# Optimization experiments

Hardware: AMD Instinct MI355X
Metric: run time of the kernel (lower is better)

## Reference

```python
import jax, jax.numpy as jnp
import numpy as np

N_NODES = 100000
N_EDGES = 3200000
IN_CH = 256
HID = 256   # 2 * out_channels
OUT = 128


def _gcn_norm(edge_index, n):
    # PyG GCNConv normalization: add self-loops, norm = d^-1/2[src] * d^-1/2[dst]
    src, dst = edge_index[0], edge_index[1]
    loops = jnp.arange(n, dtype=src.dtype)
    src = jnp.concatenate([src, loops])
    dst = jnp.concatenate([dst, loops])
    ones = jnp.ones_like(dst, dtype=jnp.float32)
    deg = jax.ops.segment_sum(ones, dst, num_segments=n)
    dinv = jnp.where(deg > 0, jax.lax.rsqrt(deg), 0.0)
    norm = dinv[src] * dinv[dst]
    return src, dst, norm


def _gcn_conv(x, W, b, src, dst, norm, n):
    h = x @ W                              # [N, F_out] dense transform first (F_out <= F_in)
    msg = h[src] * norm[:, None]           # gather + scale  [E+N, F_out]
    out = jax.ops.segment_sum(msg, dst, num_segments=n)  # scatter-add
    return out + b


def setup_inputs() -> dict:
    key = jax.random.key(0)
    k1, k2, k3, k4 = jax.random.split(key, 4)
    x = jax.random.normal(k1, (N_NODES, IN_CH), dtype=jnp.float32)
    edge_index = jax.random.randint(k2, (2, N_EDGES), 0, N_NODES, dtype=jnp.int64)
    # Glorot-style init for weights, zero bias (PyG GCNConv defaults)
    W1 = jax.random.normal(k3, (IN_CH, HID), dtype=jnp.float32) * (1.0 / np.sqrt(IN_CH))
    b1 = jnp.zeros((HID,), dtype=jnp.float32)
    W2 = jax.random.normal(k4, (HID, OUT), dtype=jnp.float32) * (1.0 / np.sqrt(HID))
    b2 = jnp.zeros((OUT,), dtype=jnp.float32)
    return {"x": x, "edge_index": edge_index, "W1": W1, "b1": b1, "W2": W2, "b2": b2}


def reference(x, edge_index, W1, b1, W2, b2):
    n = x.shape[0]
    src, dst, norm = _gcn_norm(edge_index, n)  # cached=True: shared across both layers
    h = _gcn_conv(x, W1, b1, src, dst, norm, n)
    h = jax.nn.relu(h)
    z = _gcn_conv(h, W2, b2, src, dst, norm, n)
    return z
```

## Files before the change

kernel.cpp:

```cpp
#include <hip/hip_runtime.h>
#include <cstdio>


#define NPB 256
#define PCHUNK 8192

typedef _Float16 half4v __attribute__((ext_vector_type(4)));
typedef _Float16 half8v __attribute__((ext_vector_type(8)));
typedef float    f32x4  __attribute__((ext_vector_type(4)));
typedef float    f32x8  __attribute__((ext_vector_type(8)));

__global__ __launch_bounds__(256) void k_bhist(const int* __restrict__ dst,
                                               int* __restrict__ bcnt,
                                               int e, int nb) {
  __shared__ int h[512];
  for (int i = threadIdx.x; i < nb; i += 256) h[i] = 0;
  __syncthreads();
  int c0 = blockIdx.x * PCHUNK;
  int c1 = min(c0 + PCHUNK, e);
  for (int i = c0 + threadIdx.x; i < c1; i += 256)
    atomicAdd(&h[dst[i] >> 8], 1);
  __syncthreads();
  for (int i = threadIdx.x; i < nb; i += 256)
    if (h[i]) atomicAdd(&bcnt[i], h[i]);
}

__global__ __launch_bounds__(512) void k_bscan(const int* __restrict__ bcnt,
                                               int* __restrict__ bbase,
                                               int* __restrict__ gcur, int nb) {
  __shared__ int sm[512];
  int tid = threadIdx.x;
  sm[tid] = (tid < nb) ? bcnt[tid] : 0;
  __syncthreads();
  for (int d = 1; d < 512; d <<= 1) {
    int t = (tid >= d) ? sm[tid - d] : 0;
    __syncthreads();
    sm[tid] += t;
    __syncthreads();
  }
  int ex = (tid == 0) ? 0 : sm[tid - 1];
  if (tid < nb) {
    bbase[tid] = ex;
    gcur[tid] = ex;
  }
  if (tid == nb) bbase[nb] = sm[nb - 1];
}

__global__ __launch_bounds__(256) void k_partition(const int* __restrict__ src,
                                                   const int* __restrict__ dst,
                                                   int* __restrict__ gcur,
                                                   uint2* __restrict__ tmp,
                                                   int e, int nb) {
  __shared__ int hist[512];
  __shared__ int base[512];
  for (int i = threadIdx.x; i < nb; i += 256) hist[i] = 0;
  __syncthreads();
  int c0 = blockIdx.x * PCHUNK;
  int c1 = min(c0 + PCHUNK, e);
  for (int i = c0 + threadIdx.x; i < c1; i += 256)
    atomicAdd(&hist[dst[i] >> 8], 1);
  __syncthreads();
  for (int i = threadIdx.x; i < nb; i += 256) {
    int c = hist[i];
    base[i] = c ? atomicAdd(&gcur[i], c) : 0;
    hist[i] = 0;
  }
  __syncthreads();
  for (int i = c0 + threadIdx.x; i < c1; i += 256) {
    int d = dst[i];
    int b = d >> 8;
    int pos = base[b] + atomicAdd(&hist[b], 1);
    uint2 v;
    v.x = (unsigned)src[i];
    v.y = (unsigned)d;
    tmp[pos] = v;
  }
}

__global__ __launch_bounds__(256) void k_bucket(const uint2* __restrict__ tmp,
                                                const int* __restrict__ bbase,
                                                int* __restrict__ off,
                                                float* __restrict__ dinv,
                                                int* __restrict__ esrc, int n) {
  __shared__ int lcnt[NPB];
  __shared__ int lsum[NPB];
  __shared__ int lcur[NPB];
  const int b = blockIdx.x;
  const int tid = threadIdx.x;
  const int r0 = b << 8;
  const int nn = min(NPB, n - r0);
  const int lo = bbase[b], hi = bbase[b + 1];

  lcnt[tid] = 0;
  __syncthreads();
  for (int i = lo + tid; i < hi; i += 256)
    atomicAdd(&lcnt[tmp[i].y & (NPB - 1)], 1);
  __syncthreads();
  lsum[tid] = lcnt[tid];
  __syncthreads();
  for (int d = 1; d < NPB; d <<= 1) {
    int t = (tid >= d) ? lsum[tid - d] : 0;
    __syncthreads();
    lsum[tid] += t;
    __syncthreads();
  }
  int ex = (tid == 0) ? 0 : lsum[tid - 1];
  if (tid < nn) {
    off[r0 + tid] = lo + ex;
    dinv[r0 + tid] = rsqrtf((float)(lcnt[tid] + 1));
    lcur[tid] = lo + ex;
  }
  if (r0 + nn == n && tid == 0) off[n] = hi;
  __syncthreads();
  for (int i = lo + tid; i < hi; i += 256) {
    uint2 t2 = tmp[i];
    int pos = atomicAdd(&lcur[t2.y & (NPB - 1)], 1);
    esrc[pos] = (int)t2.x;
  }
}

__global__ __launch_bounds__(256) void k_castWT(const float* __restrict__ W,
                                                _Float16* __restrict__ WhT,
                                                _Float16* __restrict__ WlT,
                                                int K, int N) {
  int i = blockIdx.x * 256 + threadIdx.x;
  if (i >= K * N) return;
  int n = i % N, k = i / N;
  float v = W[i];
  _Float16 h = (_Float16)v;
  WhT[(size_t)n * K + k] = h;
  WlT[(size_t)n * K + k] = (_Float16)(v - (float)h);
}

__global__ __launch_bounds__(256, 2) void k_gemm1(
    const float* __restrict__ A, const _Float16* __restrict__ BhT,
    const _Float16* __restrict__ BlT, _Float16* __restrict__ C,
    int M, int N, int K) {
  __shared__ _Float16 Ah[128][40];
  __shared__ _Float16 Al[128][40];

  const int tid = threadIdx.x;
  const int bm = blockIdx.x * 128;

  const int arow = tid >> 1;
  const int acol = (tid & 1) * 16;
  const bool avalid = (bm + arow) < M;
  const float* aptr = A + (size_t)(bm + arow) * K + acol;

  const int wave = tid >> 6, lane = tid & 63;
  const int wm = (wave & 1) * 64, wn = (wave >> 1) * 128;
  const int lr = lane & 15, quad = lane >> 4;

  const _Float16* bh0 = BhT + (size_t)(wn + lr) * K + quad * 8;
  const _Float16* bl0 = BlT + (size_t)(wn + lr) * K + quad * 8;

  f32x4 acc[4][8] = {};

  for (int k0 = 0; k0 < K; k0 += 32) {
    __syncthreads();
    if (avalid) {
#pragma unroll
      for (int ii = 0; ii < 4; ++ii) {
        f32x4 v = *(const f32x4*)(aptr + k0 + ii * 4);
        half4v hv, lv;
#pragma unroll
        for (int j = 0; j < 4; ++j) {
          hv[j] = (_Float16)v[j];
          lv[j] = (_Float16)(v[j] - (float)hv[j]);
        }
        *(half4v*)&Ah[arow][acol + ii * 4] = hv;
        *(half4v*)&Al[arow][acol + ii * 4] = lv;
      }
    } else {
      half4v z = {};
#pragma unroll
      for (int ii = 0; ii < 4; ++ii) {
        *(half4v*)&Ah[arow][acol + ii * 4] = z;
        *(half4v*)&Al[arow][acol + ii * 4] = z;
      }
    }
    __syncthreads();

    half8v af[4], alf[4];
#pragma unroll
    for (int mi = 0; mi < 4; ++mi) {
      af[mi] = *(const half8v*)&Ah[wm + mi * 16 + lr][quad * 8];
      alf[mi] = *(const half8v*)&Al[wm + mi * 16 + lr][quad * 8];
    }
#pragma unroll
    for (int ni = 0; ni < 8; ++ni) {
      half8v bh = *(const half8v*)(bh0 + (size_t)(ni * 16) * K + k0);
      half8v bl = *(const half8v*)(bl0 + (size_t)(ni * 16) * K + k0);
#pragma unroll
      for (int mi = 0; mi < 4; ++mi) {
        acc[mi][ni] = __builtin_amdgcn_mfma_f32_16x16x32_f16(
            af[mi], bh, acc[mi][ni], 0, 0, 0);
        acc[mi][ni] = __builtin_amdgcn_mfma_f32_16x16x32_f16(
            af[mi], bl, acc[mi][ni], 0, 0, 0);
        acc[mi][ni] = __builtin_amdgcn_mfma_f32_16x16x32_f16(
            alf[mi], bh, acc[mi][ni], 0, 0, 0);
      }
    }
  }

#pragma unroll
  for (int mi = 0; mi < 4; ++mi)
#pragma unroll
    for (int r = 0; r < 4; ++r) {
      int row = bm + wm + mi * 16 + quad * 4 + r;
      if (row < M) {
#pragma unroll
        for (int ni = 0; ni < 8; ++ni)
          C[(size_t)row * N + wn + ni * 16 + lr] = (_Float16)acc[mi][ni][r];
      }
    }
}

template <typename AT, int NTERMS>
__global__ __launch_bounds__(256, 2) void k_gemm_mfma(
    const AT* __restrict__ A, const _Float16* __restrict__ BhT,
    const _Float16* __restrict__ BlT, _Float16* __restrict__ C,
    int M, int N, int K) {
  constexpr bool SPLITA = (NTERMS == 3);
  __shared__ _Float16 Ah[128][40];
  __shared__ _Float16 Al[SPLITA ? 128 : 1][40];

  const int tid = threadIdx.x;
  const int bm = blockIdx.x * 128;
  const int bn = blockIdx.y * 128;

  const int arow = tid >> 1;
  const int acol = (tid & 1) * 16;
  const bool avalid = (bm + arow) < M;
  const AT* aptr = A + (size_t)(bm + arow) * K + acol;

  const int wave = tid >> 6, lane = tid & 63;
  const int wm = (wave & 1) * 64, wn = (wave >> 1) * 64;
  const int lr = lane & 15, quad = lane >> 4;

  const _Float16* bh0 = BhT + (size_t)(bn + wn + lr) * K + quad * 8;
  const _Float16* bl0 = BlT + (size_t)(bn + wn + lr) * K + quad * 8;

  f32x4 acc[4][4] = {};

  for (int k0 = 0; k0 < K; k0 += 32) {
    __syncthreads();
    if (avalid) {
#pragma unroll
      for (int ii = 0; ii < 4; ++ii) {
        if constexpr (SPLITA) {
          f32x4 v = *(const f32x4*)(aptr + k0 + ii * 4);
          half4v hv, lv;
#pragma unroll
          for (int j = 0; j < 4; ++j) {
            hv[j] = (_Float16)v[j];
            lv[j] = (_Float16)(v[j] - (float)hv[j]);
          }
          *(half4v*)&Ah[arow][acol + ii * 4] = hv;
          *(half4v*)&Al[arow][acol + ii * 4] = lv;
        } else {
          half4v v = *(const half4v*)(aptr + k0 + ii * 4);
          *(half4v*)&Ah[arow][acol + ii * 4] = v;
        }
      }
    } else {
      half4v z = {};
#pragma unroll
      for (int ii = 0; ii < 4; ++ii) {
        *(half4v*)&Ah[arow][acol + ii * 4] = z;
        if constexpr (SPLITA) *(half4v*)&Al[arow][acol + ii * 4] = z;
      }
    }
    __syncthreads();

    half8v af[4], alf[4], bhf[4], blf[4];
#pragma unroll
    for (int mi = 0; mi < 4; ++mi) {
      af[mi] = *(const half8v*)&Ah[wm + mi * 16 + lr][quad * 8];
      if constexpr (SPLITA)
        alf[mi] = *(const half8v*)&Al[wm + mi * 16 + lr][quad * 8];
    }
#pragma unroll
    for (int ni = 0; ni < 4; ++ni) {
      bhf[ni] = *(const half8v*)(bh0 + (size_t)(ni * 16) * K + k0);
      blf[ni] = *(const half8v*)(bl0 + (size_t)(ni * 16) * K + k0);
    }
#pragma unroll
    for (int mi = 0; mi < 4; ++mi)
#pragma unroll
      for (int ni = 0; ni < 4; ++ni) {
        acc[mi][ni] = __builtin_amdgcn_mfma_f32_16x16x32_f16(
            af[mi], bhf[ni], acc[mi][ni], 0, 0, 0);
        acc[mi][ni] = __builtin_amdgcn_mfma_f32_16x16x32_f16(
            af[mi], blf[ni], acc[mi][ni], 0, 0, 0);
        if constexpr (SPLITA)
          acc[mi][ni] = __builtin_amdgcn_mfma_f32_16x16x32_f16(
              alf[mi], bhf[ni], acc[mi][ni], 0, 0, 0);
      }
  }

#pragma unroll
  for (int mi = 0; mi < 4; ++mi)
#pragma unroll
    for (int r = 0; r < 4; ++r) {
      int row = bm + wm + mi * 16 + quad * 4 + r;
      if (row < M) {
#pragma unroll
        for (int ni = 0; ni < 4; ++ni)
          C[(size_t)row * N + bn + wn + ni * 16 + lr] =
              (_Float16)acc[mi][ni][r];
      }
    }
}

template <int C, bool RELU, typename OutT>
__global__ __launch_bounds__(256) void k_agg(const _Float16* __restrict__ h,
                                             const int* __restrict__ esrc,
                                             const int* __restrict__ off,
                                             const float* __restrict__ dinv,
                                             const float* __restrict__ bias,
                                             OutT* __restrict__ out, int n) {
  constexpr int LPE = C / 8;
  constexpr int EPL = 64 / LPE;
  constexpr int U = 4;
  int gwave = (blockIdx.x * 256 + threadIdx.x) >> 6;
  int lane = threadIdx.x & 63;
  if (gwave >= n) return;
  const int i = gwave;
  const int eslot = lane / LPE;
  const int sub = lane % LPE;
  const float di = dinv[i];
  const _Float16* hb = h + sub * 8;

  f32x8 acc = {};
  if (eslot == 0)
    acc = di * __builtin_convertvector(*(const half8v*)(hb + (size_t)i * C),
                                       f32x8);

  int e = off[i];
  const int e1 = off[i + 1];
  for (; e + U * EPL <= e1; e += U * EPL) {
    int s[U];
#pragma unroll
    for (int g = 0; g < U; ++g) s[g] = esrc[e + g * EPL + eslot];
    float w[U];
    half8v v[U];
#pragma unroll
    for (int g = 0; g < U; ++g) {
      w[g] = dinv[s[g]];
      v[g] = *(const half8v*)(hb + (size_t)s[g] * C);
    }
#pragma unroll
    for (int g = 0; g < U; ++g)
      acc += w[g] * __builtin_convertvector(v[g], f32x8);
  }
  for (; e < e1; e += EPL) {
    int eg = e + eslot;
    if (eg < e1) {
      int s = esrc[eg];
      acc += dinv[s] * __builtin_convertvector(
                           *(const half8v*)(hb + (size_t)s * C), f32x8);
    }
  }

#pragma unroll
  for (int j = 0; j < 8; ++j) {
    float t = acc[j];
#pragma unroll
    for (int m = LPE; m < 64; m <<= 1) t += __shfl_xor(t, m);
    acc[j] = t;
  }

  if (eslot == 0) {
    f32x8 bv = *(const f32x8*)(bias + sub * 8);
    f32x8 r = acc * di + bv;
    if (RELU) {
#pragma unroll
      for (int j = 0; j < 8; ++j) r[j] = fmaxf(r[j], 0.f);
    }
    if constexpr (sizeof(OutT) == 2) {
      *(half8v*)(out + (size_t)i * C + sub * 8) =
          __builtin_convertvector(r, half8v);
    } else {
      *(f32x8*)(out + (size_t)i * C + sub * 8) = r;
    }
  }
}

extern "C" void kernel_launch(void* const* d_in, const int* in_sizes, int n_in,
                              void* d_out, int out_size, void* d_ws, size_t ws_size,
                              hipStream_t stream) {
  const float* x  = (const float*)d_in[0];
  const int*   ei = (const int*)d_in[1];
  const float* W1 = (const float*)d_in[2];
  const float* b1 = (const float*)d_in[3];
  const float* W2 = (const float*)d_in[4];
  const float* b2 = (const float*)d_in[5];
  float* out = (float*)d_out;

  const int IN_CH = 256, HID = 256, OUT = 128;
  const int N = in_sizes[0] / IN_CH;
  const int E = in_sizes[1] / 2;
  const int* src = ei;
  const int* dst = ei + E;
  const int NB = (N + NPB - 1) / NPB;

  char* p = (char*)d_ws;
  auto alloc = [&](size_t bytes) {
    void* r = (void*)p;
    p += (bytes + 255) & ~(size_t)255;
    return r;
  };
  _Float16* h1   = (_Float16*)alloc((size_t)N * HID * 2);
  _Float16* h1r  = (_Float16*)alloc((size_t)N * HID * 2);
  int*      esrc = (int*)alloc((size_t)E * 4);
  uint2*    tmp  = (uint2*)alloc((size_t)E * 8);
  int*      off  = (int*)alloc((size_t)(N + 1) * 4);
  float*    dinv = (float*)alloc((size_t)N * 4);
  int*      bcnt = (int*)alloc((size_t)(NB + 1) * 4);
  int*      bbase= (int*)alloc((size_t)(NB + 1) * 4);
  int*      gcur = (int*)alloc((size_t)(NB + 1) * 4);
  _Float16* w1h  = (_Float16*)alloc((size_t)IN_CH * HID * 2);
  _Float16* w1l  = (_Float16*)alloc((size_t)IN_CH * HID * 2);
  _Float16* w2h  = (_Float16*)alloc((size_t)HID * OUT * 2);
  _Float16* w2l  = (_Float16*)alloc((size_t)HID * OUT * 2);
  if ((size_t)(p - (char*)d_ws) > ws_size) {
    fprintf(stderr, "kernel_launch: ws too small (need %zu, have %zu)\n",
            (size_t)(p - (char*)d_ws), ws_size);
    return;
  }

  const int nBlkP = (E + PCHUNK - 1) / PCHUNK;

  hipMemsetAsync(bcnt, 0, (size_t)(NB + 1) * 4, stream);
  k_bhist<<<nBlkP, 256, 0, stream>>>(dst, bcnt, E, NB);
  k_bscan<<<1, 512, 0, stream>>>(bcnt, bbase, gcur, NB);
  k_partition<<<nBlkP, 256, 0, stream>>>(src, dst, gcur, tmp, E, NB);
  k_bucket<<<NB, 256, 0, stream>>>(tmp, bbase, off, dinv, esrc, N);
  k_castWT<<<(IN_CH * HID + 255) / 256, 256, 0, stream>>>(W1, w1h, w1l, IN_CH, HID);
  k_castWT<<<(HID * OUT + 255) / 256, 256, 0, stream>>>(W2, w2h, w2l, HID, OUT);
  k_gemm1<<<(N + 127) / 128, 256, 0, stream>>>(x, w1h, w1l, h1, N, HID, IN_CH);
  int aggBlk = (N + 3) / 4;
  k_agg<256, true, _Float16><<<aggBlk, 256, 0, stream>>>(h1, esrc, off, dinv, b1, h1r, N);
  dim3 g2((N + 127) / 128, OUT / 128);
  k_gemm_mfma<_Float16, 2><<<g2, 256, 0, stream>>>(h1r, w2h, w2l, h1, N, OUT, HID);
  k_agg<128, false, float><<<aggBlk, 256, 0, stream>>>(h1, esrc, off, dinv, b2, out, N);
}
```

Baseline: 744.3 us.

## Slice edges by source range and aggregate per slice for gather locality

Edges are bucketed by source-node slice (4096 nodes) and destination block, so each slice gets its own CSR offsets. The aggregation kernel gives each wave 33 destination nodes and walks slice by slice, so the gathered source rows in each phase fall in a narrow range that should stay in cache. The wide feature dimension is split into two 128-channel passes, with each lane handling two channels. In exchange the edge-sorting histograms get much larger (about 12.5K shared-memory bins) and per-edge parallelism drops, since each lane walks edges serially with short-vector loads.

```diff
diff --git a/kernel.cpp b/kernel.cpp
--- a/kernel.cpp
+++ b/kernel.cpp
@@ -4,33 +4,45 @@
 
 #define NPB 256
 #define PCHUNK 8192
-
+#define SLICE_SHIFT 12
+#define MAXB 12544
+
+typedef _Float16 half2v __attribute__((ext_vector_type(2)));
 typedef _Float16 half4v __attribute__((ext_vector_type(4)));
 typedef _Float16 half8v __attribute__((ext_vector_type(8)));
+typedef float    f32x2  __attribute__((ext_vector_type(2)));
 typedef float    f32x4  __attribute__((ext_vector_type(4)));
-typedef float    f32x8  __attribute__((ext_vector_type(8)));
-
-__global__ __launch_bounds__(256) void k_bhist(const int* __restrict__ dst,
+
+__global__ __launch_bounds__(256) void k_bhist(const int* __restrict__ src,
+                                               const int* __restrict__ dst,
                                                int* __restrict__ bcnt,
-                                               int e, int nb) {
-  __shared__ int h[512];
-  for (int i = threadIdx.x; i < nb; i += 256) h[i] = 0;
+                                               int e, int nb, int nb2) {
+  __shared__ int h[MAXB];
+  for (int i = threadIdx.x; i < nb2; i += 256) h[i] = 0;
   __syncthreads();
   int c0 = blockIdx.x * PCHUNK;
   int c1 = min(c0 + PCHUNK, e);
-  for (int i = c0 + threadIdx.x; i < c1; i += 256)
-    atomicAdd(&h[dst[i] >> 8], 1);
-  __syncthreads();
-  for (int i = threadIdx.x; i < nb; i += 256)
+  for (int i = c0 + threadIdx.x; i < c1; i += 256) {
+    int key = ((unsigned)src[i] >> SLICE_SHIFT) * nb + ((unsigned)dst[i] >> 8);
+    atomicAdd(&h[key], 1);
+  }
+  __syncthreads();
+  for (int i = threadIdx.x; i < nb2; i += 256)
     if (h[i]) atomicAdd(&bcnt[i], h[i]);
 }
 
-__global__ __launch_bounds__(512) void k_bscan(const int* __restrict__ bcnt,
-                                               int* __restrict__ bbase,
-                                               int* __restrict__ gcur, int nb) {
+__global__ __launch_bounds__(512) void k_bscan2(const int* __restrict__ bcnt,
+                                                int* __restrict__ bbase,
+                                                int* __restrict__ gcur,
+                                                int nb2) {
   __shared__ int sm[512];
-  int tid = threadIdx.x;
-  sm[tid] = (tid < nb) ? bcnt[tid] : 0;
+  const int tid = threadIdx.x;
+  const int chunk = (nb2 + 511) >> 9;
+  const int c0 = min(tid * chunk, nb2);
+  const int c1 = min(c0 + chunk, nb2);
+  int sum = 0;
+  for (int j = c0; j < c1; ++j) sum += bcnt[j];
+  sm[tid] = sum;
   __syncthreads();
   for (int d = 1; d < 512; d <<= 1) {
     int t = (tid >= d) ? sm[tid - d] : 0;
@@ -38,40 +50,41 @@
     sm[tid] += t;
     __syncthreads();
   }
-  int ex = (tid == 0) ? 0 : sm[tid - 1];
-  if (tid < nb) {
-    bbase[tid] = ex;
-    gcur[tid] = ex;
-  }
-  if (tid == nb) bbase[nb] = sm[nb - 1];
+  int run = (tid == 0) ? 0 : sm[tid - 1];
+  for (int j = c0; j < c1; ++j) {
+    bbase[j] = run;
+    gcur[j] = run;
+    run += bcnt[j];
+  }
+  if (tid == 511) bbase[nb2] = run;
 }
 
 __global__ __launch_bounds__(256) void k_partition(const int* __restrict__ src,
                                                    const int* __restrict__ dst,
                                                    int* __restrict__ gcur,
                                                    uint2* __restrict__ tmp,
-                                                   int e, int nb) {
-  __shared__ int hist[512];
-  __shared__ int base[512];
-  for (int i = threadIdx.x; i < nb; i += 256) hist[i] = 0;
+                                                   int e, int nb, int nb2) {
+  __shared__ int hist[MAXB];
+  for (int i = threadIdx.x; i < nb2; i += 256) hist[i] = 0;
   __syncthreads();
   int c0 = blockIdx.x * PCHUNK;
   int c1 = min(c0 + PCHUNK, e);
-  for (int i = c0 + threadIdx.x; i < c1; i += 256)
-    atomicAdd(&hist[dst[i] >> 8], 1);
-  __syncthreads();
-  for (int i = threadIdx.x; i < nb; i += 256) {
+  for (int i = c0 + threadIdx.x; i < c1; i += 256) {
+    int key = ((unsigned)src[i] >> SLICE_SHIFT) * nb + ((unsigned)dst[i] >> 8);
+    atomicAdd(&hist[key], 1);
+  }
+  __syncthreads();
+  for (int i = threadIdx.x; i < nb2; i += 256) {
     int c = hist[i];
-    base[i] = c ? atomicAdd(&gcur[i], c) : 0;
-    hist[i] = 0;
+    hist[i] = c ? atomicAdd(&gcur[i], c) : 0;
   }
   __syncthreads();
   for (int i = c0 + threadIdx.x; i < c1; i += 256) {
-    int d = dst[i];
-    int b = d >> 8;
-    int pos = base[b] + atomicAdd(&hist[b], 1);
+    int s = src[i], d = dst[i];
+    int key = ((unsigned)s >> SLICE_SHIFT) * nb + ((unsigned)d >> 8);
+    int pos = atomicAdd(&hist[key], 1);
     uint2 v;
-    v.x = (unsigned)src[i];
+    v.x = (unsigned)s;
     v.y = (unsigned)d;
     tmp[pos] = v;
   }
@@ -79,15 +92,14 @@
 
 __global__ __launch_bounds__(256) void k_bucket(const uint2* __restrict__ tmp,
                                                 const int* __restrict__ bbase,
-                                                int* __restrict__ off,
-                                                float* __restrict__ dinv,
+                                                int* __restrict__ off2,
                                                 int* __restrict__ esrc, int n) {
   __shared__ int lcnt[NPB];
   __shared__ int lsum[NPB];
   __shared__ int lcur[NPB];
-  const int b = blockIdx.x;
+  const int b = blockIdx.y * gridDim.x + blockIdx.x;
   const int tid = threadIdx.x;
-  const int r0 = b << 8;
+  const int r0 = blockIdx.x << 8;
   const int nn = min(NPB, n - r0);
   const int lo = bbase[b], hi = bbase[b + 1];
 
@@ -106,17 +118,28 @@
   }
   int ex = (tid == 0) ? 0 : lsum[tid - 1];
   if (tid < nn) {
-    off[r0 + tid] = lo + ex;
-    dinv[r0 + tid] = rsqrtf((float)(lcnt[tid] + 1));
+    off2[(size_t)blockIdx.y * n + r0 + tid] = lo + ex;
     lcur[tid] = lo + ex;
   }
-  if (r0 + nn == n && tid == 0) off[n] = hi;
+  if (blockIdx.y == gridDim.y - 1 && r0 + nn == n && tid == 0)
+    off2[(size_t)gridDim.y * n] = hi;
   __syncthreads();
   for (int i = lo + tid; i < hi; i += 256) {
     uint2 t2 = tmp[i];
     int pos = atomicAdd(&lcur[t2.y & (NPB - 1)], 1);
     esrc[pos] = (int)t2.x;
   }
+}
+
+__global__ __launch_bounds__(256) void k_deg(const int* __restrict__ off2,
+                                             float* __restrict__ dinv,
+                                             int n, int nslice) {
+  int i = blockIdx.x * 256 + threadIdx.x;
+  if (i >= n) return;
+  int deg = 0;
+  for (int s = 0; s < nslice; ++s)
+    deg += off2[(size_t)s * n + i + 1] - off2[(size_t)s * n + i];
+  dinv[i] = rsqrtf((float)(deg + 1));
 }
 
 __global__ __launch_bounds__(256) void k_castWT(const float* __restrict__ W,
@@ -313,76 +336,101 @@
     }
 }
 
-template <int C, bool RELU, typename OutT>
-__global__ __launch_bounds__(256) void k_agg(const _Float16* __restrict__ h,
-                                             const int* __restrict__ esrc,
-                                             const int* __restrict__ off,
-                                             const float* __restrict__ dinv,
-                                             const float* __restrict__ bias,
-                                             OutT* __restrict__ out, int n) {
-  constexpr int LPE = C / 8;
-  constexpr int EPL = 64 / LPE;
-  constexpr int U = 4;
-  int gwave = (blockIdx.x * 256 + threadIdx.x) >> 6;
-  int lane = threadIdx.x & 63;
-  if (gwave >= n) return;
-  const int i = gwave;
-  const int eslot = lane / LPE;
-  const int sub = lane % LPE;
-  const float di = dinv[i];
-  const _Float16* hb = h + sub * 8;
-
-  f32x8 acc = {};
-  if (eslot == 0)
-    acc = di * __builtin_convertvector(*(const half8v*)(hb + (size_t)i * C),
-                                       f32x8);
-
-  int e = off[i];
-  const int e1 = off[i + 1];
-  for (; e + U * EPL <= e1; e += U * EPL) {
-    int s[U];
-#pragma unroll
-    for (int g = 0; g < U; ++g) s[g] = esrc[e + g * EPL + eslot];
-    float w[U];
-    half8v v[U];
-#pragma unroll
-    for (int g = 0; g < U; ++g) {
-      w[g] = dinv[s[g]];
-      v[g] = *(const half8v*)(hb + (size_t)s[g] * C);
-    }
-#pragma unroll
-    for (int g = 0; g < U; ++g)
-      acc += w[g] * __builtin_convertvector(v[g], f32x8);
-  }
-  for (; e < e1; e += EPL) {
-    int eg = e + eslot;
-    if (eg < e1) {
-      int s = esrc[eg];
-      acc += dinv[s] * __builtin_convertvector(
-                           *(const half8v*)(hb + (size_t)s * C), f32x8);
-    }
-  }
-
-#pragma unroll
-  for (int j = 0; j < 8; ++j) {
-    float t = acc[j];
-#pragma unroll
-    for (int m = LPE; m < 64; m <<= 1) t += __shfl_xor(t, m);
-    acc[j] = t;
-  }
-
-  if (eslot == 0) {
-    f32x8 bv = *(const f32x8*)(bias + sub * 8);
-    f32x8 r = acc * di + bv;
-    if (RELU) {
-#pragma unroll
-      for (int j = 0; j < 8; ++j) r[j] = fmaxf(r[j], 0.f);
-    }
-    if constexpr (sizeof(OutT) == 2) {
-      *(half8v*)(out + (size_t)i * C + sub * 8) =
-          __builtin_convertvector(r, half8v);
-    } else {
-      *(f32x8*)(out + (size_t)i * C + sub * 8) = r;
+template <int CS, bool RELU, typename OutT>
+__global__ __launch_bounds__(256, 3) void k_agg_sl(
+    const _Float16* __restrict__ h, const int* __restrict__ esrc,
+    const int* __restrict__ off2, const float* __restrict__ dinv,
+    const float* __restrict__ bias, OutT* __restrict__ out,
+    int n, int nslice, int chbase) {
+  constexpr int NPW = 33;
+  const int gwave = blockIdx.x * 4 + (threadIdx.x >> 6);
+  const int lane = threadIdx.x & 63;
+  const int i0 = gwave * NPW;
+  const int ch = chbase + lane * 2;
+  const _Float16* hb = h + ch;
+
+  f32x2 acc[NPW];
+#pragma unroll
+  for (int nd = 0; nd < NPW; ++nd) {
+    int i = i0 + nd;
+    acc[nd] = (f32x2){0.f, 0.f};
+    if (i < n)
+      acc[nd] = dinv[i] * __builtin_convertvector(
+                              *(const half2v*)(hb + (size_t)i * CS), f32x2);
+  }
+
+  for (int s = 0; s < nslice; ++s) {
+    const int* o = off2 + (size_t)s * n;
+#pragma unroll
+    for (int c = 0; c < NPW; c += 8) {
+      int e0[8], e1[8], sv[8];
+      float w[8];
+      half2v hv[8];
+#pragma unroll
+      for (int j = 0; j < 8; ++j) {
+        e0[j] = 0;
+        e1[j] = 0;
+        if (c + j < NPW) {
+          int i = i0 + c + j;
+          if (i < n) {
+            e0[j] = o[i];
+            e1[j] = o[i + 1];
+          }
+        }
+      }
+#pragma unroll
+      for (int j = 0; j < 8; ++j) sv[j] = (e0[j] < e1[j]) ? esrc[e0[j]] : -1;
+#pragma unroll
+      for (int j = 0; j < 8; ++j)
+        if (sv[j] >= 0) {
+          w[j] = dinv[sv[j]];
+          hv[j] = *(const half2v*)(hb + (size_t)sv[j] * CS);
+        }
+#pragma unroll
+      for (int j = 0; j < 8; ++j)
+        if (c + j < NPW && sv[j] >= 0)
+          acc[c + j] += w[j] * __builtin_convertvector(hv[j], f32x2);
+#pragma unroll
+      for (int j = 0; j < 8; ++j)
+        sv[j] = (e0[j] + 1 < e1[j]) ? esrc[e0[j] + 1] : -1;
+#pragma unroll
+      for (int j = 0; j < 8; ++j)
+        if (sv[j] >= 0) {
+          w[j] = dinv[sv[j]];
+          hv[j] = *(const half2v*)(hb + (size_t)sv[j] * CS);
+        }
+#pragma unroll
+      for (int j = 0; j < 8; ++j)
+        if (c + j < NPW && sv[j] >= 0)
+          acc[c + j] += w[j] * __builtin_convertvector(hv[j], f32x2);
+#pragma unroll
+      for (int j = 0; j < 8; ++j)
+        if (c + j < NPW)
+          for (int e = e0[j] + 2; e < e1[j]; ++e) {
+            int v2 = esrc[e];
+            acc[c + j] +=
+                dinv[v2] * __builtin_convertvector(
+                               *(const half2v*)(hb + (size_t)v2 * CS), f32x2);
+          }
+    }
+  }
+
+#pragma unroll
+  for (int nd = 0; nd < NPW; ++nd) {
+    int i = i0 + nd;
+    if (i < n) {
+      f32x2 bv = *(const f32x2*)(bias + ch);
+      f32x2 r = acc[nd] * dinv[i] + bv;
+      if (RELU) {
+        r[0] = fmaxf(r[0], 0.f);
+        r[1] = fmaxf(r[1], 0.f);
+      }
+      if constexpr (sizeof(OutT) == 2) {
+        *(half2v*)(out + (size_t)i * CS + ch) =
+            __builtin_convertvector(r, half2v);
+      } else {
+        *(f32x2*)(out + (size_t)i * CS + ch) = r;
+      }
     }
   }
 }
@@ -404,6 +452,8 @@
   const int* src = ei;
   const int* dst = ei + E;
   const int NB = (N + NPB - 1) / NPB;
+  const int NSLICE = (N + (1 << SLICE_SHIFT) - 1) >> SLICE_SHIFT;
+  const int nb2 = NSLICE * NB;
 
   char* p = (char*)d_ws;
   auto alloc = [&](size_t bytes) {
@@ -415,11 +465,11 @@
   _Float16* h1r  = (_Float16*)alloc((size_t)N * HID * 2);
   int*      esrc = (int*)alloc((size_t)E * 4);
   uint2*    tmp  = (uint2*)alloc((size_t)E * 8);
-  int*      off  = (int*)alloc((size_t)(N + 1) * 4);
+  int*      off2 = (int*)alloc(((size_t)NSLICE * N + 1) * 4);
   float*    dinv = (float*)alloc((size_t)N * 4);
-  int*      bcnt = (int*)alloc((size_t)(NB + 1) * 4);
-  int*      bbase= (int*)alloc((size_t)(NB + 1) * 4);
-  int*      gcur = (int*)alloc((size_t)(NB + 1) * 4);
+  int*      bcnt = (int*)alloc((size_t)(nb2 + 1) * 4);
+  int*      bbase= (int*)alloc((size_t)(nb2 + 1) * 4);
+  int*      gcur = (int*)alloc((size_t)(nb2 + 1) * 4);
   _Float16* w1h  = (_Float16*)alloc((size_t)IN_CH * HID * 2);
   _Float16* w1l  = (_Float16*)alloc((size_t)IN_CH * HID * 2);
   _Float16* w2h  = (_Float16*)alloc((size_t)HID * OUT * 2);
@@ -432,17 +482,22 @@
 
   const int nBlkP = (E + PCHUNK - 1) / PCHUNK;
 
-  hipMemsetAsync(bcnt, 0, (size_t)(NB + 1) * 4, stream);
-  k_bhist<<<nBlkP, 256, 0, stream>>>(dst, bcnt, E, NB);
-  k_bscan<<<1, 512, 0, stream>>>(bcnt, bbase, gcur, NB);
-  k_partition<<<nBlkP, 256, 0, stream>>>(src, dst, gcur, tmp, E, NB);
-  k_bucket<<<NB, 256, 0, stream>>>(tmp, bbase, off, dinv, esrc, N);
+  hipMemsetAsync(bcnt, 0, (size_t)(nb2 + 1) * 4, stream);
+  k_bhist<<<nBlkP, 256, 0, stream>>>(src, dst, bcnt, E, NB, nb2);
+  k_bscan2<<<1, 512, 0, stream>>>(bcnt, bbase, gcur, nb2);
+  k_partition<<<nBlkP, 256, 0, stream>>>(src, dst, gcur, tmp, E, NB, nb2);
+  k_bucket<<<dim3(NB, NSLICE), 256, 0, stream>>>(tmp, bbase, off2, esrc, N);
+  k_deg<<<(N + 255) / 256, 256, 0, stream>>>(off2, dinv, N, NSLICE);
   k_castWT<<<(IN_CH * HID + 255) / 256, 256, 0, stream>>>(W1, w1h, w1l, IN_CH, HID);
   k_castWT<<<(HID * OUT + 255) / 256, 256, 0, stream>>>(W2, w2h, w2l, HID, OUT);
   k_gemm1<<<(N + 127) / 128, 256, 0, stream>>>(x, w1h, w1l, h1, N, HID, IN_CH);
-  int aggBlk = (N + 3) / 4;
-  k_agg<256, true, _Float16><<<aggBlk, 256, 0, stream>>>(h1, esrc, off, dinv, b1, h1r, N);
+  const int aggBlk = (N + 4 * 33 - 1) / (4 * 33);
+  k_agg_sl<256, true, _Float16><<<aggBlk, 256, 0, stream>>>(
+      h1, esrc, off2, dinv, b1, h1r, N, NSLICE, 0);
+  k_agg_sl<256, true, _Float16><<<aggBlk, 256, 0, stream>>>(
+      h1, esrc, off2, dinv, b1, h1r, N, NSLICE, 128);
   dim3 g2((N + 127) / 128, OUT / 128);
   k_gemm_mfma<_Float16, 2><<<g2, 256, 0, stream>>>(h1r, w2h, w2l, h1, N, OUT, HID);
-  k_agg<128, false, float><<<aggBlk, 256, 0, stream>>>(h1, esrc, off, dinv, b2, out, N);
-}
+  k_agg_sl<128, false, float><<<aggBlk, 256, 0, stream>>>(
+      h1, esrc, off2, dinv, b2, out, N, NSLICE, 0);
+}
```

Result: slower. 1.593 ms (+114.0%).

## Pre-split X into fp16 hi/lo and load GEMM A fragments directly from global

Applied to the files above, without the earlier changes.

A separate kernel now casts X into fp16 high and low parts up front, and it writes them into workspace buffers that are reused (an aliased temp slice and h1r). Both GEMMs drop the LDS staging and the __syncthreads, and each wave loads its A fragments straight from global memory. This removes barrier and LDS traffic and the repeated conversion work inside the GEMM. In exchange it adds an extra pass over X (read fp32, write two fp16 copies) and uses uncoalesced strided global loads for A that rely on caching.

```diff
diff --git a/kernel.cpp b/kernel.cpp
--- a/kernel.cpp
+++ b/kernel.cpp
@@ -132,60 +132,51 @@
   WlT[(size_t)n * K + k] = (_Float16)(v - (float)h);
 }
 
-__global__ __launch_bounds__(256, 2) void k_gemm1(
-    const float* __restrict__ A, const _Float16* __restrict__ BhT,
-    const _Float16* __restrict__ BlT, _Float16* __restrict__ C,
-    int M, int N, int K) {
-  __shared__ _Float16 Ah[128][40];
-  __shared__ _Float16 Al[128][40];
-
+__global__ __launch_bounds__(256) void k_castX(const float* __restrict__ X,
+                                               _Float16* __restrict__ Xh,
+                                               _Float16* __restrict__ Xl,
+                                               int total4) {
+  int i = blockIdx.x * 256 + threadIdx.x;
+  if (i >= total4) return;
+  f32x4 v = *(const f32x4*)(X + (size_t)i * 4);
+  half4v h, l;
+#pragma unroll
+  for (int j = 0; j < 4; ++j) {
+    h[j] = (_Float16)v[j];
+    l[j] = (_Float16)(v[j] - (float)h[j]);
+  }
+  *(half4v*)(Xh + (size_t)i * 4) = h;
+  *(half4v*)(Xl + (size_t)i * 4) = l;
+}
+
+__global__ __launch_bounds__(256, 2) void k_gemm1d(
+    const _Float16* __restrict__ Ah, const _Float16* __restrict__ Al,
+    const _Float16* __restrict__ BhT, const _Float16* __restrict__ BlT,
+    _Float16* __restrict__ C, int M, int N, int K) {
   const int tid = threadIdx.x;
   const int bm = blockIdx.x * 128;
-
-  const int arow = tid >> 1;
-  const int acol = (tid & 1) * 16;
-  const bool avalid = (bm + arow) < M;
-  const float* aptr = A + (size_t)(bm + arow) * K + acol;
-
   const int wave = tid >> 6, lane = tid & 63;
   const int wm = (wave & 1) * 64, wn = (wave >> 1) * 128;
   const int lr = lane & 15, quad = lane >> 4;
 
+  const _Float16 *a0[4], *l0[4];
+#pragma unroll
+  for (int mi = 0; mi < 4; ++mi) {
+    int row = bm + wm + mi * 16 + lr;
+    row = row < M ? row : M - 1;
+    a0[mi] = Ah + (size_t)row * K + quad * 8;
+    l0[mi] = Al + (size_t)row * K + quad * 8;
+  }
   const _Float16* bh0 = BhT + (size_t)(wn + lr) * K + quad * 8;
   const _Float16* bl0 = BlT + (size_t)(wn + lr) * K + quad * 8;
 
   f32x4 acc[4][8] = {};
-
   for (int k0 = 0; k0 < K; k0 += 32) {
-    __syncthreads();
-    if (avalid) {
-#pragma unroll
-      for (int ii = 0; ii < 4; ++ii) {
-        f32x4 v = *(const f32x4*)(aptr + k0 + ii * 4);
-        half4v hv, lv;
-#pragma unroll
-        for (int j = 0; j < 4; ++j) {
-          hv[j] = (_Float16)v[j];
-          lv[j] = (_Float16)(v[j] - (float)hv[j]);
-        }
-        *(half4v*)&Ah[arow][acol + ii * 4] = hv;
-        *(half4v*)&Al[arow][acol + ii * 4] = lv;
-      }
-    } else {
-      half4v z = {};
-#pragma unroll
-      for (int ii = 0; ii < 4; ++ii) {
-        *(half4v*)&Ah[arow][acol + ii * 4] = z;
-        *(half4v*)&Al[arow][acol + ii * 4] = z;
-      }
-    }
-    __syncthreads();
-
     half8v af[4], alf[4];
 #pragma unroll
     for (int mi = 0; mi < 4; ++mi) {
-      af[mi] = *(const half8v*)&Ah[wm + mi * 16 + lr][quad * 8];
-      alf[mi] = *(const half8v*)&Al[wm + mi * 16 + lr][quad * 8];
+      af[mi] = *(const half8v*)(a0[mi] + k0);
+      alf[mi] = *(const half8v*)(l0[mi] + k0);
     }
 #pragma unroll
     for (int ni = 0; ni < 8; ++ni) {
@@ -216,87 +207,43 @@
     }
 }
 
-template <typename AT, int NTERMS>
-__global__ __launch_bounds__(256, 2) void k_gemm_mfma(
-    const AT* __restrict__ A, const _Float16* __restrict__ BhT,
+__global__ __launch_bounds__(256, 2) void k_gemm2d(
+    const _Float16* __restrict__ A, const _Float16* __restrict__ BhT,
     const _Float16* __restrict__ BlT, _Float16* __restrict__ C,
     int M, int N, int K) {
-  constexpr bool SPLITA = (NTERMS == 3);
-  __shared__ _Float16 Ah[128][40];
-  __shared__ _Float16 Al[SPLITA ? 128 : 1][40];
-
   const int tid = threadIdx.x;
   const int bm = blockIdx.x * 128;
-  const int bn = blockIdx.y * 128;
-
-  const int arow = tid >> 1;
-  const int acol = (tid & 1) * 16;
-  const bool avalid = (bm + arow) < M;
-  const AT* aptr = A + (size_t)(bm + arow) * K + acol;
-
   const int wave = tid >> 6, lane = tid & 63;
   const int wm = (wave & 1) * 64, wn = (wave >> 1) * 64;
   const int lr = lane & 15, quad = lane >> 4;
 
-  const _Float16* bh0 = BhT + (size_t)(bn + wn + lr) * K + quad * 8;
-  const _Float16* bl0 = BlT + (size_t)(bn + wn + lr) * K + quad * 8;
+  const _Float16* a0[4];
+#pragma unroll
+  for (int mi = 0; mi < 4; ++mi) {
+    int row = bm + wm + mi * 16 + lr;
+    row = row < M ? row : M - 1;
+    a0[mi] = A + (size_t)row * K + quad * 8;
+  }
+  const _Float16* bh0 = BhT + (size_t)(wn + lr) * K + quad * 8;
+  const _Float16* bl0 = BlT + (size_t)(wn + lr) * K + quad * 8;
 
   f32x4 acc[4][4] = {};
-
   for (int k0 = 0; k0 < K; k0 += 32) {
-    __syncthreads();
-    if (avalid) {
-#pragma unroll
-      for (int ii = 0; ii < 4; ++ii) {
-        if constexpr (SPLITA) {
-          f32x4 v = *(const f32x4*)(aptr + k0 + ii * 4);
-          half4v hv, lv;
-#pragma unroll
-          for (int j = 0; j < 4; ++j) {
-            hv[j] = (_Float16)v[j];
-            lv[j] = (_Float16)(v[j] - (float)hv[j]);
-          }
-          *(half4v*)&Ah[arow][acol + ii * 4] = hv;
-          *(half4v*)&Al[arow][acol + ii * 4] = lv;
-        } else {
-          half4v v = *(const half4v*)(aptr + k0 + ii * 4);
-          *(half4v*)&Ah[arow][acol + ii * 4] = v;
-        }
+    half8v af[4];
+#pragma unroll
+    for (int mi = 0; mi < 4; ++mi) af[mi] = *(const half8v*)(a0[mi] + k0);
+#pragma unroll
+    for (int ni = 0; ni < 4; ++ni) {
+      half8v bh = *(const half8v*)(bh0 + (size_t)(ni * 16) * K + k0);
+      half8v bl = *(const half8v*)(bl0 + (size_t)(ni * 16) * K + k0);
+#pragma unroll
+      for (int mi = 0; mi < 4; ++mi) {
+        acc[mi][ni] = __builtin_amdgcn_mfma_f32_16x16x32_f16(
+            af[mi], bh, acc[mi][ni], 0, 0, 0);
+        acc[mi][ni] = __builtin_amdgcn_mfma_f32_16x16x32_f16(
+            af[mi], bl, acc[mi][ni], 0, 0, 0);
       }
-    } else {
-      half4v z = {};
-#pragma unroll
-      for (int ii = 0; ii < 4; ++ii) {
-        *(half4v*)&Ah[arow][acol + ii * 4] = z;
-        if constexpr (SPLITA) *(half4v*)&Al[arow][acol + ii * 4] = z;
-      }
-    }
-    __syncthreads();
-
-    half8v af[4], alf[4], bhf[4], blf[4];
-#pragma unroll
-    for (int mi = 0; mi < 4; ++mi) {
-      af[mi] = *(const half8v*)&Ah[wm + mi * 16 + lr][quad * 8];
-      if constexpr (SPLITA)
-        alf[mi] = *(const half8v*)&Al[wm + mi * 16 + lr][quad * 8];
-    }
-#pragma unroll
-    for (int ni = 0; ni < 4; ++ni) {
-      bhf[ni] = *(const half8v*)(bh0 + (size_t)(ni * 16) * K + k0);
-      blf[ni] = *(const half8v*)(bl0 + (size_t)(ni * 16) * K + k0);
-    }
-#pragma unroll
-    for (int mi = 0; mi < 4; ++mi)
-#pragma unroll
-      for (int ni = 0; ni < 4; ++ni) {
-        acc[mi][ni] = __builtin_amdgcn_mfma_f32_16x16x32_f16(
-            af[mi], bhf[ni], acc[mi][ni], 0, 0, 0);
-        acc[mi][ni] = __builtin_amdgcn_mfma_f32_16x16x32_f16(
-            af[mi], blf[ni], acc[mi][ni], 0, 0, 0);
-        if constexpr (SPLITA)
-          acc[mi][ni] = __builtin_amdgcn_mfma_f32_16x16x32_f16(
-              alf[mi], bhf[ni], acc[mi][ni], 0, 0, 0);
-      }
+    }
   }
 
 #pragma unroll
@@ -307,8 +254,7 @@
       if (row < M) {
 #pragma unroll
         for (int ni = 0; ni < 4; ++ni)
-          C[(size_t)row * N + bn + wn + ni * 16 + lr] =
-              (_Float16)acc[mi][ni][r];
+          C[(size_t)row * N + wn + ni * 16 + lr] = (_Float16)acc[mi][ni][r];
       }
     }
 }
@@ -414,7 +360,6 @@
   _Float16* h1   = (_Float16*)alloc((size_t)N * HID * 2);
   _Float16* h1r  = (_Float16*)alloc((size_t)N * HID * 2);
   int*      esrc = (int*)alloc((size_t)E * 4);
-  uint2*    tmp  = (uint2*)alloc((size_t)E * 8);
   int*      off  = (int*)alloc((size_t)(N + 1) * 4);
   float*    dinv = (float*)alloc((size_t)N * 4);
   int*      bcnt = (int*)alloc((size_t)(NB + 1) * 4);
@@ -424,11 +369,17 @@
   _Float16* w1l  = (_Float16*)alloc((size_t)IN_CH * HID * 2);
   _Float16* w2h  = (_Float16*)alloc((size_t)HID * OUT * 2);
   _Float16* w2l  = (_Float16*)alloc((size_t)HID * OUT * 2);
+  size_t sliceBytes = (size_t)E * 8;
+  size_t xlBytes = (size_t)N * IN_CH * 2;
+  char*  sliceA = (char*)alloc(sliceBytes > xlBytes ? sliceBytes : xlBytes);
   if ((size_t)(p - (char*)d_ws) > ws_size) {
     fprintf(stderr, "kernel_launch: ws too small (need %zu, have %zu)\n",
             (size_t)(p - (char*)d_ws), ws_size);
     return;
   }
+  uint2*    tmp = (uint2*)sliceA;
+  _Float16* xl  = (_Float16*)sliceA;
+  _Float16* xh  = h1r;
 
   const int nBlkP = (E + PCHUNK - 1) / PCHUNK;
 
@@ -439,10 +390,12 @@
   k_bucket<<<NB, 256, 0, stream>>>(tmp, bbase, off, dinv, esrc, N);
   k_castWT<<<(IN_CH * HID + 255) / 256, 256, 0, stream>>>(W1, w1h, w1l, IN_CH, HID);
   k_castWT<<<(HID * OUT + 255) / 256, 256, 0, stream>>>(W2, w2h, w2l, HID, OUT);
-  k_gemm1<<<(N + 127) / 128, 256, 0, stream>>>(x, w1h, w1l, h1, N, HID, IN_CH);
+  k_castX<<<(N * IN_CH / 4 + 255) / 256, 256, 0, stream>>>(
+      x, xh, xl, N * IN_CH / 4);
+  k_gemm1d<<<(N + 127) / 128, 256, 0, stream>>>(xh, xl, w1h, w1l, h1,
+                                                N, HID, IN_CH);
   int aggBlk = (N + 3) / 4;
   k_agg<256, true, _Float16><<<aggBlk, 256, 0, stream>>>(h1, esrc, off, dinv, b1, h1r, N);
-  dim3 g2((N + 127) / 128, OUT / 128);
-  k_gemm_mfma<_Float16, 2><<<g2, 256, 0, stream>>>(h1r, w2h, w2l, h1, N, OUT, HID);
+  k_gemm2d<<<(N + 127) / 128, 256, 0, stream>>>(h1r, w2h, w2l, h1, N, OUT, HID);
   k_agg<128, false, float><<<aggBlk, 256, 0, stream>>>(h1, esrc, off, dinv, b2, out, N);
 }
```

New measurement: 794.2 us. 6.7% more time.

## Simplify CSR build with global atomics and split aggregation into 64-channel passes

Applied to the files above, without the earlier changes.

The two-level bucketed partition that built the CSR is replaced by three simpler kernels: a global-atomic degree count, a single-block scan that writes offsets and dinv, and an atomic-cursor scatter of source indices. This removes the 8-byte temporary edge buffer and two passes over it. The price is contended random global atomics and a serial single-workgroup scan over 100k nodes. Aggregation now runs as several launches that each cover only a 64-channel slice of the features. The aim is a smaller per-pass gather working set that caches better, at the cost of re-reading the edge lists and dinv once per pass.

```diff
diff --git a/kernel.cpp b/kernel.cpp
--- a/kernel.cpp
+++ b/kernel.cpp
@@ -1,122 +1,59 @@
 #include <hip/hip_runtime.h>
 #include <cstdio>
 
-
-#define NPB 256
-#define PCHUNK 8192
 
 typedef _Float16 half4v __attribute__((ext_vector_type(4)));
 typedef _Float16 half8v __attribute__((ext_vector_type(8)));
 typedef float    f32x4  __attribute__((ext_vector_type(4)));
 typedef float    f32x8  __attribute__((ext_vector_type(8)));
 
-__global__ __launch_bounds__(256) void k_bhist(const int* __restrict__ dst,
-                                               int* __restrict__ bcnt,
-                                               int e, int nb) {
-  __shared__ int h[512];
-  for (int i = threadIdx.x; i < nb; i += 256) h[i] = 0;
+__global__ __launch_bounds__(256) void k_deg(const int* __restrict__ dst,
+                                             int* __restrict__ deg, int e) {
+  int i = blockIdx.x * 256 + threadIdx.x;
+  if (i < e) atomicAdd(&deg[dst[i]], 1);
+}
+
+__global__ __launch_bounds__(1024) void k_scan(const int* __restrict__ deg,
+                                               int* __restrict__ off,
+                                               int* __restrict__ gcur,
+                                               float* __restrict__ dinv,
+                                               int n) {
+  __shared__ int sm[1024];
+  const int tid = threadIdx.x;
+  const int chunk = (n + 1 + 1023) >> 10;
+  const int c0 = min(tid * chunk, n + 1);
+  const int c1 = min(c0 + chunk, n + 1);
+  int sum = 0;
+  for (int j = c0; j < c1; ++j)
+    if (j < n) sum += deg[j];
+  sm[tid] = sum;
   __syncthreads();
-  int c0 = blockIdx.x * PCHUNK;
-  int c1 = min(c0 + PCHUNK, e);
-  for (int i = c0 + threadIdx.x; i < c1; i += 256)
-    atomicAdd(&h[dst[i] >> 8], 1);
-  __syncthreads();
-  for (int i = threadIdx.x; i < nb; i += 256)
-    if (h[i]) atomicAdd(&bcnt[i], h[i]);
-}
-
-__global__ __launch_bounds__(512) void k_bscan(const int* __restrict__ bcnt,
-                                               int* __restrict__ bbase,
-                                               int* __restrict__ gcur, int nb) {
-  __shared__ int sm[512];
-  int tid = threadIdx.x;
-  sm[tid] = (tid < nb) ? bcnt[tid] : 0;
-  __syncthreads();
-  for (int d = 1; d < 512; d <<= 1) {
+  for (int d = 1; d < 1024; d <<= 1) {
     int t = (tid >= d) ? sm[tid - d] : 0;
     __syncthreads();
     sm[tid] += t;
     __syncthreads();
   }
-  int ex = (tid == 0) ? 0 : sm[tid - 1];
-  if (tid < nb) {
-    bbase[tid] = ex;
-    gcur[tid] = ex;
-  }
-  if (tid == nb) bbase[nb] = sm[nb - 1];
-}
-
-__global__ __launch_bounds__(256) void k_partition(const int* __restrict__ src,
-                                                   const int* __restrict__ dst,
-                                                   int* __restrict__ gcur,
-                                                   uint2* __restrict__ tmp,
-                                                   int e, int nb) {
-  __shared__ int hist[512];
-  __shared__ int base[512];
-  for (int i = threadIdx.x; i < nb; i += 256) hist[i] = 0;
-  __syncthreads();
-  int c0 = blockIdx.x * PCHUNK;
-  int c1 = min(c0 + PCHUNK, e);
-  for (int i = c0 + threadIdx.x; i < c1; i += 256)
-    atomicAdd(&hist[dst[i] >> 8], 1);
-  __syncthreads();
-  for (int i = threadIdx.x; i < nb; i += 256) {
-    int c = hist[i];
-    base[i] = c ? atomicAdd(&gcur[i], c) : 0;
-    hist[i] = 0;
-  }
-  __syncthreads();
-  for (int i = c0 + threadIdx.x; i < c1; i += 256) {
-    int d = dst[i];
-    int b = d >> 8;
-    int pos = base[b] + atomicAdd(&hist[b], 1);
-    uint2 v;
-    v.x = (unsigned)src[i];
-    v.y = (unsigned)d;
-    tmp[pos] = v;
-  }
-}
-
-__global__ __launch_bounds__(256) void k_bucket(const uint2* __restrict__ tmp,
-                                                const int* __restrict__ bbase,
-                                                int* __restrict__ off,
-                                                float* __restrict__ dinv,
-                                                int* __restrict__ esrc, int n) {
-  __shared__ int lcnt[NPB];
-  __shared__ int lsum[NPB];
-  __shared__ int lcur[NPB];
-  const int b = blockIdx.x;
-  const int tid = threadIdx.x;
-  const int r0 = b << 8;
-  const int nn = min(NPB, n - r0);
-  const int lo = bbase[b], hi = bbase[b + 1];
-
-  lcnt[tid] = 0;
-  __syncthreads();
-  for (int i = lo + tid; i < hi; i += 256)
-    atomicAdd(&lcnt[tmp[i].y & (NPB - 1)], 1);
-  __syncthreads();
-  lsum[tid] = lcnt[tid];
-  __syncthreads();
-  for (int d = 1; d < NPB; d <<= 1) {
-    int t = (tid >= d) ? lsum[tid - d] : 0;
-    __syncthreads();
-    lsum[tid] += t;
-    __syncthreads();
-  }
-  int ex = (tid == 0) ? 0 : lsum[tid - 1];
-  if (tid < nn) {
-    off[r0 + tid] = lo + ex;
-    dinv[r0 + tid] = rsqrtf((float)(lcnt[tid] + 1));
-    lcur[tid] = lo + ex;
-  }
-  if (r0 + nn == n && tid == 0) off[n] = hi;
-  __syncthreads();
-  for (int i = lo + tid; i < hi; i += 256) {
-    uint2 t2 = tmp[i];
-    int pos = atomicAdd(&lcur[t2.y & (NPB - 1)], 1);
-    esrc[pos] = (int)t2.x;
-  }
+  int run = (tid == 0) ? 0 : sm[tid - 1];
+  for (int j = c0; j < c1; ++j) {
+    off[j] = run;
+    if (j < n) {
+      gcur[j] = run;
+      dinv[j] = rsqrtf((float)(deg[j] + 1));
+      run += deg[j];
+    }
+  }
+}
+
+__global__ __launch_bounds__(256) void k_scatter(const int* __restrict__ src,
+                                                 const int* __restrict__ dst,
+                                                 int* __restrict__ gcur,
+                                                 int* __restrict__ esrc,
+                                                 int e) {
+  int i = blockIdx.x * 256 + threadIdx.x;
+  if (i >= e) return;
+  int pos = atomicAdd(&gcur[dst[i]], 1);
+  esrc[pos] = src[i];
 }
 
 __global__ __launch_bounds__(256) void k_castWT(const float* __restrict__ W,
@@ -313,14 +250,15 @@
     }
 }
 
-template <int C, bool RELU, typename OutT>
+template <int C, int CPP, bool RELU, typename OutT>
 __global__ __launch_bounds__(256) void k_agg(const _Float16* __restrict__ h,
                                              const int* __restrict__ esrc,
                                              const int* __restrict__ off,
                                              const float* __restrict__ dinv,
                                              const float* __restrict__ bias,
-                                             OutT* __restrict__ out, int n) {
-  constexpr int LPE = C / 8;
+                                             OutT* __restrict__ out, int n,
+                                             int pass) {
+  constexpr int LPE = CPP / 8;
   constexpr int EPL = 64 / LPE;
   constexpr int U = 4;
   int gwave = (blockIdx.x * 256 + threadIdx.x) >> 6;
@@ -330,7 +268,7 @@
   const int eslot = lane / LPE;
   const int sub = lane % LPE;
   const float di = dinv[i];
-  const _Float16* hb = h + sub * 8;
+  const _Float16* hb = h + (size_t)pass * CPP + sub * 8;
 
   f32x8 acc = {};
   if (eslot == 0)
@@ -372,17 +310,17 @@
   }
 
   if (eslot == 0) {
-    f32x8 bv = *(const f32x8*)(bias + sub * 8);
+    f32x8 bv = *(const f32x8*)(bias + pass * CPP + sub * 8);
     f32x8 r = acc * di + bv;
     if (RELU) {
 #pragma unroll
       for (int j = 0; j < 8; ++j) r[j] = fmaxf(r[j], 0.f);
     }
     if constexpr (sizeof(OutT) == 2) {
-      *(half8v*)(out + (size_t)i * C + sub * 8) =
+      *(half8v*)(out + (size_t)i * C + pass * CPP + sub * 8) =
           __builtin_convertvector(r, half8v);
     } else {
-      *(f32x8*)(out + (size_t)i * C + sub * 8) = r;
+      *(f32x8*)(out + (size_t)i * C + pass * CPP + sub * 8) = r;
     }
   }
 }
@@ -403,7 +341,6 @@
   const int E = in_sizes[1] / 2;
   const int* src = ei;
   const int* dst = ei + E;
-  const int NB = (N + NPB - 1) / NPB;
 
   char* p = (char*)d_ws;
   auto alloc = [&](size_t bytes) {
@@ -414,12 +351,10 @@
   _Float16* h1   = (_Float16*)alloc((size_t)N * HID * 2);
   _Float16* h1r  = (_Float16*)alloc((size_t)N * HID * 2);
   int*      esrc = (int*)alloc((size_t)E * 4);
-  uint2*    tmp  = (uint2*)alloc((size_t)E * 8);
   int*      off  = (int*)alloc((size_t)(N + 1) * 4);
   float*    dinv = (float*)alloc((size_t)N * 4);
-  int*      bcnt = (int*)alloc((size_t)(NB + 1) * 4);
-  int*      bbase= (int*)alloc((size_t)(NB + 1) * 4);
-  int*      gcur = (int*)alloc((size_t)(NB + 1) * 4);
+  int*      deg  = (int*)alloc((size_t)N * 4);
+  int*      gcur = (int*)alloc((size_t)N * 4);
   _Float16* w1h  = (_Float16*)alloc((size_t)IN_CH * HID * 2);
   _Float16* w1l  = (_Float16*)alloc((size_t)IN_CH * HID * 2);
   _Float16* w2h  = (_Float16*)alloc((size_t)HID * OUT * 2);
@@ -430,19 +365,22 @@
     return;
   }
 
-  const int nBlkP = (E + PCHUNK - 1) / PCHUNK;
-
-  hipMemsetAsync(bcnt, 0, (size_t)(NB + 1) * 4, stream);
-  k_bhist<<<nBlkP, 256, 0, stream>>>(dst, bcnt, E, NB);
-  k_bscan<<<1, 512, 0, stream>>>(bcnt, bbase, gcur, NB);
-  k_partition<<<nBlkP, 256, 0, stream>>>(src, dst, gcur, tmp, E, NB);
-  k_bucket<<<NB, 256, 0, stream>>>(tmp, bbase, off, dinv, esrc, N);
+  const int eBlk = (E + 255) / 256;
+
+  hipMemsetAsync(deg, 0, (size_t)N * 4, stream);
+  k_deg<<<eBlk, 256, 0, stream>>>(dst, deg, E);
+  k_scan<<<1, 1024, 0, stream>>>(deg, off, gcur, dinv, N);
+  k_scatter<<<eBlk, 256, 0, stream>>>(src, dst, gcur, esrc, E);
   k_castWT<<<(IN_CH * HID + 255) / 256, 256, 0, stream>>>(W1, w1h, w1l, IN_CH, HID);
   k_castWT<<<(HID * OUT + 255) / 256, 256, 0, stream>>>(W2, w2h, w2l, HID, OUT);
   k_gemm1<<<(N + 127) / 128, 256, 0, stream>>>(x, w1h, w1l, h1, N, HID, IN_CH);
   int aggBlk = (N + 3) / 4;
-  k_agg<256, true, _Float16><<<aggBlk, 256, 0, stream>>>(h1, esrc, off, dinv, b1, h1r, N);
+  for (int pass = 0; pass < 4; ++pass)
+    k_agg<256, 64, true, _Float16><<<aggBlk, 256, 0, stream>>>(
+        h1, esrc, off, dinv, b1, h1r, N, pass);
   dim3 g2((N + 127) / 128, OUT / 128);
   k_gemm_mfma<_Float16, 2><<<g2, 256, 0, stream>>>(h1r, w2h, w2l, h1, N, OUT, HID);
-  k_agg<128, false, float><<<aggBlk, 256, 0, stream>>>(h1, esrc, off, dinv, b2, out, N);
-}
+  for (int pass = 0; pass < 2; ++pass)
+    k_agg<128, 64, false, float><<<aggBlk, 256, 0, stream>>>(
+        h1, esrc, off, dinv, b2, out, N, pass);
+}
```

Result: slower. 1.360 ms (+82.7%).
